# Performance work log

Hardware: AMD Instinct MI355X
Metric: run time of the kernel (lower is better)

Reference implementation:

```python
import jax, jax.numpy as jnp
import numpy as np


def setup_inputs() -> dict:
    key = jax.random.key(0)
    ks = jax.random.split(key, 6)
    B_, S, D, N = 8, 4096, 1024, 16
    return {
        "x": jax.random.normal(ks[0], (B_, S, D), dtype=jnp.float32),
        "A": jax.random.normal(ks[1], (N, N), dtype=jnp.float32),
        "B": jax.random.normal(ks[2], (D, N), dtype=jnp.float32),
        "C": jax.random.normal(ks[3], (N, D), dtype=jnp.float32),
        "W_out": jax.random.normal(ks[4], (D, D), dtype=jnp.float32) * 0.02,
        "b_out": jax.random.normal(ks[5], (D,), dtype=jnp.float32) * 0.02,
    }


def reference(x, A, B, C, W_out, b_out):
    # x: [batch, seq, d_model]. Recurrence: h_t = tanh(x_t @ B + h_{t-1} @ A.T)
    # Precompute the input projection for all timesteps (the only large GEMM),
    # then scan the tiny d_state-wide recurrence over time.
    xB = jnp.einsum("bsd,dn->sbn", x, B)  # [seq, batch, d_state]
    h0 = jnp.zeros((x.shape[0], A.shape[0]), dtype=x.dtype)

    def step(h, xb_t):
        h = jnp.tanh(xb_t + h @ A.T)
        return h, h

    _, hs = jax.lax.scan(step, h0, xB)  # hs: [seq, batch, d_state]
    y = jnp.einsum("sbn,nd->bsd", hs, C)  # [batch, seq, d_model]
    # proj_out (torch Linear): y @ W.T + b
    return y @ W_out.T + b_out
```

## Files before the change

kernel.cpp:

```cpp
#include <hip/hip_runtime.h>
#include <math.h>

#define B_DIM 8
#define S_DIM 4096
#define D_DIM 1024
#define N_DIM 16
#define ROWS (B_DIM * S_DIM)

#define CHUNK_L 32
#define WARM 64
#define STEPS (CHUNK_L + WARM)
#define NCHAIN (B_DIM * (S_DIM / CHUNK_L))

#define TILE_R 64
#define TILE_K 64
#define XB_BLOCKS (ROWS / TILE_R)
#define CW_BLOCKS ((N_DIM * D_DIM) / 256)

__global__ __launch_bounds__(256) void k_xbcw(const float* __restrict__ x,
                                              const float* __restrict__ Bm,
                                              float* __restrict__ xb,
                                              const float* __restrict__ C,
                                              const float* __restrict__ W,
                                              float* __restrict__ CW) {
    const int t = threadIdx.x;
    if (blockIdx.x >= XB_BLOCKS) {
        int u = (blockIdx.x - XB_BLOCKS) * 256 + t;
        int d = u >> 4;
        int n = u & 15;
        const float* crow = C + n * D_DIM;
        const float* wrow = W + (size_t)d * D_DIM;
        float acc = 0.f;
#pragma unroll 4
        for (int k = 0; k < D_DIM; k += 4) {
            float4 c4 = *(const float4*)(crow + k);
            float4 w4 = *(const float4*)(wrow + k);
            acc = fmaf(c4.x, w4.x, acc);
            acc = fmaf(c4.y, w4.y, acc);
            acc = fmaf(c4.z, w4.z, acc);
            acc = fmaf(c4.w, w4.w, acc);
        }
        CW[n * D_DIM + d] = acc;
        return;
    }
    __shared__ float xs[TILE_R][68];
    __shared__ float bs[TILE_K][20];
    const int row0 = blockIdx.x * TILE_R;
    const int row = t >> 2;
    const int nq = (t & 3) * 4;
    float4 acc = {0.f, 0.f, 0.f, 0.f};

    for (int kc = 0; kc < D_DIM; kc += TILE_K) {
#pragma unroll
        for (int p = 0; p < 4; ++p) {
            int fid = p * 256 + t;
            int r = fid >> 4;
            int q = (fid & 15) * 4;
            float4 v = *(const float4*)(x + (size_t)(row0 + r) * D_DIM + kc + q);
            xs[r][q + 0] = v.x; xs[r][q + 1] = v.y;
            xs[r][q + 2] = v.z; xs[r][q + 3] = v.w;
        }
        {
            int r = t >> 2;
            int q = (t & 3) * 4;
            float4 v = *(const float4*)(Bm + (size_t)(kc + r) * N_DIM + q);
            bs[r][q + 0] = v.x; bs[r][q + 1] = v.y;
            bs[r][q + 2] = v.z; bs[r][q + 3] = v.w;
        }
        __syncthreads();
#pragma unroll 8
        for (int kk = 0; kk < TILE_K; ++kk) {
            float xv = xs[row][kk];
            acc.x = fmaf(xv, bs[kk][nq + 0], acc.x);
            acc.y = fmaf(xv, bs[kk][nq + 1], acc.y);
            acc.z = fmaf(xv, bs[kk][nq + 2], acc.z);
            acc.w = fmaf(xv, bs[kk][nq + 3], acc.w);
        }
        __syncthreads();
    }
    *(float4*)(xb + (size_t)(row0 + row) * N_DIM + nq) = acc;
}

__global__ __launch_bounds__(64) void k_scan(const float* __restrict__ xb,
                                             const float* __restrict__ A,
                                             float* __restrict__ hs) {
    const int tid = threadIdx.x;
    const int n = tid & 15;
    const int base4 = (tid & 48) * 4;

    const int chain = blockIdx.x * 4 + (tid >> 4);
    const int b = chain >> 7;
    const int chunk = chain & 127;
    const int t0 = chunk * CHUNK_L - WARM;

    float Ar[16];
#pragma unroll
    for (int m4 = 0; m4 < 16; m4 += 4) {
        float4 v = *(const float4*)(A + n * 16 + m4);
        Ar[m4 + 0] = v.x; Ar[m4 + 1] = v.y; Ar[m4 + 2] = v.z; Ar[m4 + 3] = v.w;
    }

    const float* xp = xb + (size_t)b * S_DIM * N_DIM + n;
    float* hp = hs + (size_t)b * S_DIM * N_DIM + n;

    float ring[8];
#pragma unroll
    for (int i = 0; i < 8; ++i) {
        int tt = t0 + i;
        ring[i] = (tt >= 0) ? xp[(size_t)tt * N_DIM] : 0.f;
    }

    float h = 0.f;
    for (int tr0 = 0; tr0 < STEPS; tr0 += 8) {
#pragma unroll
        for (int j = 0; j < 8; ++j) {
            const int tr = tr0 + j;
            const float xv = ring[j];
            const int hbits = __float_as_int(h);
            int hm[16];
#pragma unroll
            for (int m = 0; m < 16; ++m)
                hm[m] = __builtin_amdgcn_ds_bpermute(base4 + m * 4, hbits);
            float acc0 = xv, acc1 = 0.f;
#pragma unroll
            for (int m = 0; m < 8; ++m) {
                acc0 = fmaf(Ar[m], __int_as_float(hm[m]), acc0);
                acc1 = fmaf(Ar[m + 8], __int_as_float(hm[m + 8]), acc1);
            }
            float g = acc0 + acc1;
            float ax = fabsf(g);
            float e = __expf(2.f * ax);
            float tv = 1.f - 2.f / (e + 1.f);
            h = (g < 0.f) ? -tv : tv;
            if (tr >= WARM)
                hp[(size_t)(t0 + tr) * N_DIM] = h;
            int tt = t0 + tr + 8;
            if (tr + 8 < STEPS)
                ring[j] = (tt >= 0) ? xp[(size_t)tt * N_DIM] : 0.f;
        }
    }
}

__global__ __launch_bounds__(256) void k_out(const float* __restrict__ hs,
                                             const float* __restrict__ CW,
                                             const float* __restrict__ bias,
                                             float* __restrict__ out) {
    const int t = threadIdx.x;
    const int d0 = t * 4;
    const int row0 = blockIdx.x * 32;
    float4 cw[16];
#pragma unroll
    for (int nn = 0; nn < 16; ++nn)
        cw[nn] = *(const float4*)(CW + nn * D_DIM + d0);
    float4 b4 = *(const float4*)(bias + d0);

    for (int r = row0; r < row0 + 32; ++r) {
        const float4* hp = (const float4*)(hs + (size_t)r * N_DIM);
        float4 h0 = hp[0], h1 = hp[1], h2 = hp[2], h3 = hp[3];
        float hv[16] = {h0.x, h0.y, h0.z, h0.w, h1.x, h1.y, h1.z, h1.w,
                        h2.x, h2.y, h2.z, h2.w, h3.x, h3.y, h3.z, h3.w};
        float4 acc = b4;
#pragma unroll
        for (int nn = 0; nn < 16; ++nn) {
            acc.x = fmaf(hv[nn], cw[nn].x, acc.x);
            acc.y = fmaf(hv[nn], cw[nn].y, acc.y);
            acc.z = fmaf(hv[nn], cw[nn].z, acc.z);
            acc.w = fmaf(hv[nn], cw[nn].w, acc.w);
        }
        *(float4*)(out + (size_t)r * D_DIM + d0) = acc;
    }
}

extern "C" void kernel_launch(void* const* d_in, const int* in_sizes, int n_in,
                              void* d_out, int out_size, void* d_ws,
                              size_t ws_size, hipStream_t stream) {
    const float* x    = (const float*)d_in[0];
    const float* A    = (const float*)d_in[1];
    const float* Bm   = (const float*)d_in[2];
    const float* C    = (const float*)d_in[3];
    const float* W    = (const float*)d_in[4];
    const float* bias = (const float*)d_in[5];
    float* out = (float*)d_out;

    float* ws = (float*)d_ws;
    float* xb = ws;
    float* hs = ws + 524288;
    float* CW = ws + 1048576;

    k_xbcw<<<dim3(XB_BLOCKS + CW_BLOCKS), dim3(256), 0, stream>>>(x, Bm, xb, C, W, CW);
    k_scan<<<dim3(NCHAIN / 4), dim3(64), 0, stream>>>(xb, A, hs);
    k_out<<<dim3(ROWS / 32), dim3(256), 0, stream>>>(hs, CW, bias, out);
}
```

Baseline: 121.6 us.

## Restructure x@B GEMM as split-K with register prefetch and separate reduction

The x@B projection now splits K into four quarters across blocks. Each thread owns one row and holds all 16 output columns in registers, reads B straight from global memory as broadcast loads, and prefetches the next x chunk into registers while computing the current one. Partial sums go to a workspace, and a new reduction kernel adds them into xb. The aim is more arithmetic per shared-memory load and less synchronisation than the old 64x64 tiling. The cost is an extra launch plus the write and read of the partial sums.

```diff
diff --git a/kernel.cpp b/kernel.cpp
--- a/kernel.cpp
+++ b/kernel.cpp
@@ -12,14 +12,16 @@
 #define STEPS (CHUNK_L + WARM)
 #define NCHAIN (B_DIM * (S_DIM / CHUNK_L))
 
-#define TILE_R 64
-#define TILE_K 64
-#define XB_BLOCKS (ROWS / TILE_R)
+#define XB_BLOCKS 512
 #define CW_BLOCKS ((N_DIM * D_DIM) / 256)
+#define XROWS 256
+#define KQ 256
+#define CK 32
+#define PAD 36
 
 __global__ __launch_bounds__(256) void k_xbcw(const float* __restrict__ x,
                                               const float* __restrict__ Bm,
-                                              float* __restrict__ xb,
+                                              float* __restrict__ parts,
                                               const float* __restrict__ C,
                                               const float* __restrict__ W,
                                               float* __restrict__ CW) {
@@ -43,42 +45,85 @@
         CW[n * D_DIM + d] = acc;
         return;
     }
-    __shared__ float xs[TILE_R][68];
-    __shared__ float bs[TILE_K][20];
-    const int row0 = blockIdx.x * TILE_R;
-    const int row = t >> 2;
-    const int nq = (t & 3) * 4;
-    float4 acc = {0.f, 0.f, 0.f, 0.f};
-
-    for (int kc = 0; kc < D_DIM; kc += TILE_K) {
-#pragma unroll
-        for (int p = 0; p < 4; ++p) {
+    __shared__ float xs[XROWS * PAD];
+    const int rt = blockIdx.x >> 2;
+    const int kq = blockIdx.x & 3;
+    const int row0 = rt * XROWS;
+    const int kq0 = kq * KQ;
+    const float* xbase = x + (size_t)row0 * D_DIM + kq0;
+
+    float acc[16];
+#pragma unroll
+    for (int n = 0; n < 16; ++n) acc[n] = 0.f;
+
+    float4 pf[8];
+#pragma unroll
+    for (int p = 0; p < 8; ++p) {
+        int fid = p * 256 + t;
+        int r = fid >> 3;
+        int q = fid & 7;
+        pf[p] = *(const float4*)(xbase + (size_t)r * D_DIM + q * 4);
+    }
+
+    for (int c = 0; c < 8; ++c) {
+        __syncthreads();
+#pragma unroll
+        for (int p = 0; p < 8; ++p) {
             int fid = p * 256 + t;
-            int r = fid >> 4;
-            int q = (fid & 15) * 4;
-            float4 v = *(const float4*)(x + (size_t)(row0 + r) * D_DIM + kc + q);
-            xs[r][q + 0] = v.x; xs[r][q + 1] = v.y;
-            xs[r][q + 2] = v.z; xs[r][q + 3] = v.w;
-        }
-        {
-            int r = t >> 2;
-            int q = (t & 3) * 4;
-            float4 v = *(const float4*)(Bm + (size_t)(kc + r) * N_DIM + q);
-            bs[r][q + 0] = v.x; bs[r][q + 1] = v.y;
-            bs[r][q + 2] = v.z; bs[r][q + 3] = v.w;
+            int r = fid >> 3;
+            int q = fid & 7;
+            *(float4*)(xs + r * PAD + q * 4) = pf[p];
         }
         __syncthreads();
-#pragma unroll 8
-        for (int kk = 0; kk < TILE_K; ++kk) {
-            float xv = xs[row][kk];
-            acc.x = fmaf(xv, bs[kk][nq + 0], acc.x);
-            acc.y = fmaf(xv, bs[kk][nq + 1], acc.y);
-            acc.z = fmaf(xv, bs[kk][nq + 2], acc.z);
-            acc.w = fmaf(xv, bs[kk][nq + 3], acc.w);
-        }
-        __syncthreads();
-    }
-    *(float4*)(xb + (size_t)(row0 + row) * N_DIM + nq) = acc;
+        if (c < 7) {
+#pragma unroll
+            for (int p = 0; p < 8; ++p) {
+                int fid = p * 256 + t;
+                int r = fid >> 3;
+                int q = fid & 7;
+                pf[p] = *(const float4*)(xbase + (size_t)r * D_DIM +
+                                         (c + 1) * CK + q * 4);
+            }
+        }
+        const float* bk = Bm + (size_t)(kq0 + c * CK) * N_DIM;
+#pragma unroll
+        for (int j = 0; j < 8; ++j) {
+            float4 xv = *(const float4*)(xs + t * PAD + j * 4);
+            const float* b0 = bk + (j * 4 + 0) * N_DIM;
+            const float* b1 = bk + (j * 4 + 1) * N_DIM;
+            const float* b2 = bk + (j * 4 + 2) * N_DIM;
+            const float* b3 = bk + (j * 4 + 3) * N_DIM;
+#pragma unroll
+            for (int n = 0; n < 16; ++n) {
+                float a = acc[n];
+                a = fmaf(xv.x, b0[n], a);
+                a = fmaf(xv.y, b1[n], a);
+                a = fmaf(xv.z, b2[n], a);
+                a = fmaf(xv.w, b3[n], a);
+                acc[n] = a;
+            }
+        }
+    }
+    float* op = parts + ((size_t)kq * ROWS + row0 + t) * N_DIM;
+#pragma unroll
+    for (int j = 0; j < 4; ++j) {
+        float4 v = {acc[j * 4 + 0], acc[j * 4 + 1],
+                    acc[j * 4 + 2], acc[j * 4 + 3]};
+        *(float4*)(op + j * 4) = v;
+    }
+}
+
+__global__ __launch_bounds__(256) void k_red(const float* __restrict__ parts,
+                                             float* __restrict__ xb) {
+    int i = (blockIdx.x * 256 + threadIdx.x) * 4;
+    const size_t Q = (size_t)ROWS * N_DIM;
+    float4 a = *(const float4*)(parts + i);
+    float4 b = *(const float4*)(parts + Q + i);
+    float4 c = *(const float4*)(parts + 2 * Q + i);
+    float4 d = *(const float4*)(parts + 3 * Q + i);
+    float4 s = {(a.x + b.x) + (c.x + d.x), (a.y + b.y) + (c.y + d.y),
+                (a.z + b.z) + (c.z + d.z), (a.w + b.w) + (c.w + d.w)};
+    *(float4*)(xb + i) = s;
 }
 
 __global__ __launch_bounds__(64) void k_scan(const float* __restrict__ xb,
@@ -182,12 +227,15 @@
     const float* bias = (const float*)d_in[5];
     float* out = (float*)d_out;
 
-    float* ws = (float*)d_ws;
-    float* xb = ws;
-    float* hs = ws + 524288;
-    float* CW = ws + 1048576;
-
-    k_xbcw<<<dim3(XB_BLOCKS + CW_BLOCKS), dim3(256), 0, stream>>>(x, Bm, xb, C, W, CW);
+    float* ws    = (float*)d_ws;
+    float* xb    = ws;
+    float* hs    = ws + 524288;
+    float* CW    = ws + 1048576;
+    float* parts = ws + 1064960;
+
+    k_xbcw<<<dim3(XB_BLOCKS + CW_BLOCKS), dim3(256), 0, stream>>>(
+        x, Bm, parts, C, W, CW);
+    k_red<<<dim3(ROWS * N_DIM / 1024), dim3(256), 0, stream>>>(parts, xb);
     k_scan<<<dim3(NCHAIN / 4), dim3(64), 0, stream>>>(xb, A, hs);
     k_out<<<dim3(ROWS / 32), dim3(256), 0, stream>>>(hs, CW, bias, out);
 }
```

After: 171.0 us. 40.7% more time.

## Split-K the x@B projection with register-blocked tiles and a reduction kernel

Applied to the files above, without the earlier changes.

Replaces the shared-memory tiled x@B GEMM with a split-K version. Each block handles 512 rows by 64 k. Each thread holds 8 rows by 4 outputs in registers and double-buffers its x loads straight from global memory instead of staging them through LDS. Partial sums go to a 16-way workspace, and a new reduction kernel sums them into xb. This aims to raise memory-level parallelism and FMA density for the bandwidth-bound 128MB read of x. In exchange it adds an extra launch plus about 32MB of partial-sum traffic, and the x loads are strided across rows.

```diff
diff --git a/kernel.cpp b/kernel.cpp
--- a/kernel.cpp
+++ b/kernel.cpp
@@ -12,20 +12,21 @@
 #define STEPS (CHUNK_L + WARM)
 #define NCHAIN (B_DIM * (S_DIM / CHUNK_L))
 
-#define TILE_R 64
-#define TILE_K 64
-#define XB_BLOCKS (ROWS / TILE_R)
+#define KSPLIT 16
+#define KB 64
+#define RT2 512
+#define XB2_BLOCKS ((ROWS / RT2) * KSPLIT)
 #define CW_BLOCKS ((N_DIM * D_DIM) / 256)
 
-__global__ __launch_bounds__(256) void k_xbcw(const float* __restrict__ x,
-                                              const float* __restrict__ Bm,
-                                              float* __restrict__ xb,
-                                              const float* __restrict__ C,
-                                              const float* __restrict__ W,
-                                              float* __restrict__ CW) {
+__global__ __launch_bounds__(256, 4) void k_xbcw(const float* __restrict__ x,
+                                                 const float* __restrict__ Bm,
+                                                 float* __restrict__ parts,
+                                                 const float* __restrict__ C,
+                                                 const float* __restrict__ W,
+                                                 float* __restrict__ CW) {
     const int t = threadIdx.x;
-    if (blockIdx.x >= XB_BLOCKS) {
-        int u = (blockIdx.x - XB_BLOCKS) * 256 + t;
+    if (blockIdx.x >= XB2_BLOCKS) {
+        int u = (blockIdx.x - XB2_BLOCKS) * 256 + t;
         int d = u >> 4;
         int n = u & 15;
         const float* crow = C + n * D_DIM;
@@ -43,42 +44,87 @@
         CW[n * D_DIM + d] = acc;
         return;
     }
-    __shared__ float xs[TILE_R][68];
-    __shared__ float bs[TILE_K][20];
-    const int row0 = blockIdx.x * TILE_R;
-    const int row = t >> 2;
+    __shared__ float bs[KB * N_DIM];
+    const int rt = blockIdx.x >> 4;
+    const int ks = blockIdx.x & 15;
+    const int row0 = rt * RT2;
+    const int k0 = ks * KB;
+
+    *(float4*)(bs + t * 4) = *(const float4*)(Bm + (size_t)k0 * N_DIM + t * 4);
+    __syncthreads();
+
+    const int rg = t >> 2;
     const int nq = (t & 3) * 4;
-    float4 acc = {0.f, 0.f, 0.f, 0.f};
-
-    for (int kc = 0; kc < D_DIM; kc += TILE_K) {
-#pragma unroll
-        for (int p = 0; p < 4; ++p) {
-            int fid = p * 256 + t;
-            int r = fid >> 4;
-            int q = (fid & 15) * 4;
-            float4 v = *(const float4*)(x + (size_t)(row0 + r) * D_DIM + kc + q);
-            xs[r][q + 0] = v.x; xs[r][q + 1] = v.y;
-            xs[r][q + 2] = v.z; xs[r][q + 3] = v.w;
-        }
-        {
-            int r = t >> 2;
-            int q = (t & 3) * 4;
-            float4 v = *(const float4*)(Bm + (size_t)(kc + r) * N_DIM + q);
-            bs[r][q + 0] = v.x; bs[r][q + 1] = v.y;
-            bs[r][q + 2] = v.z; bs[r][q + 3] = v.w;
-        }
-        __syncthreads();
-#pragma unroll 8
-        for (int kk = 0; kk < TILE_K; ++kk) {
-            float xv = xs[row][kk];
-            acc.x = fmaf(xv, bs[kk][nq + 0], acc.x);
-            acc.y = fmaf(xv, bs[kk][nq + 1], acc.y);
-            acc.z = fmaf(xv, bs[kk][nq + 2], acc.z);
-            acc.w = fmaf(xv, bs[kk][nq + 3], acc.w);
-        }
-        __syncthreads();
-    }
-    *(float4*)(xb + (size_t)(row0 + row) * N_DIM + nq) = acc;
+    const float* xr = x + (size_t)(row0 + rg * 8) * D_DIM + k0;
+
+    float4 acc[8];
+#pragma unroll
+    for (int i = 0; i < 8; ++i) acc[i] = {0.f, 0.f, 0.f, 0.f};
+
+    float4 bufA[8], bufB[8];
+#pragma unroll
+    for (int i = 0; i < 8; ++i)
+        bufA[i] = *(const float4*)(xr + (size_t)i * D_DIM);
+#pragma unroll
+    for (int i = 0; i < 8; ++i)
+        bufB[i] = *(const float4*)(xr + (size_t)i * D_DIM + 4);
+
+#define FMAALL(BUF, JJ)                                                    \
+    {                                                                      \
+        const float* bk = bs + (JJ) * 4 * N_DIM + nq;                      \
+        float4 b0 = *(const float4*)(bk + 0 * N_DIM);                      \
+        float4 b1 = *(const float4*)(bk + 1 * N_DIM);                      \
+        float4 b2 = *(const float4*)(bk + 2 * N_DIM);                      \
+        float4 b3 = *(const float4*)(bk + 3 * N_DIM);                      \
+        _Pragma("unroll")                                                  \
+        for (int i = 0; i < 8; ++i) {                                      \
+            float4 xv = BUF[i];                                            \
+            float4 a = acc[i];                                             \
+            a.x = fmaf(xv.x, b0.x, a.x); a.y = fmaf(xv.x, b0.y, a.y);      \
+            a.z = fmaf(xv.x, b0.z, a.z); a.w = fmaf(xv.x, b0.w, a.w);      \
+            a.x = fmaf(xv.y, b1.x, a.x); a.y = fmaf(xv.y, b1.y, a.y);      \
+            a.z = fmaf(xv.y, b1.z, a.z); a.w = fmaf(xv.y, b1.w, a.w);      \
+            a.x = fmaf(xv.z, b2.x, a.x); a.y = fmaf(xv.z, b2.y, a.y);      \
+            a.z = fmaf(xv.z, b2.z, a.z); a.w = fmaf(xv.z, b2.w, a.w);      \
+            a.x = fmaf(xv.w, b3.x, a.x); a.y = fmaf(xv.w, b3.y, a.y);      \
+            a.z = fmaf(xv.w, b3.z, a.z); a.w = fmaf(xv.w, b3.w, a.w);      \
+            acc[i] = a;                                                    \
+        }                                                                  \
+    }
+
+    for (int j = 0; j < 16; j += 2) {
+        FMAALL(bufA, j)
+        if (j + 2 < 16) {
+#pragma unroll
+            for (int i = 0; i < 8; ++i)
+                bufA[i] = *(const float4*)(xr + (size_t)i * D_DIM + (j + 2) * 4);
+        }
+        FMAALL(bufB, j + 1)
+        if (j + 3 < 16) {
+#pragma unroll
+            for (int i = 0; i < 8; ++i)
+                bufB[i] = *(const float4*)(xr + (size_t)i * D_DIM + (j + 3) * 4);
+        }
+    }
+#undef FMAALL
+
+    float* op = parts + ((size_t)ks * ROWS + row0 + rg * 8) * N_DIM + nq;
+#pragma unroll
+    for (int i = 0; i < 8; ++i)
+        *(float4*)(op + (size_t)i * N_DIM) = acc[i];
+}
+
+__global__ __launch_bounds__(256) void k_red(const float* __restrict__ parts,
+                                             float* __restrict__ xb) {
+    int i = (blockIdx.x * 256 + threadIdx.x) * 4;
+    const size_t Q = (size_t)ROWS * N_DIM;
+    float4 s = *(const float4*)(parts + i);
+#pragma unroll
+    for (int q = 1; q < KSPLIT; ++q) {
+        float4 v = *(const float4*)(parts + (size_t)q * Q + i);
+        s.x += v.x; s.y += v.y; s.z += v.z; s.w += v.w;
+    }
+    *(float4*)(xb + i) = s;
 }
 
 __global__ __launch_bounds__(64) void k_scan(const float* __restrict__ xb,
@@ -182,12 +228,15 @@
     const float* bias = (const float*)d_in[5];
     float* out = (float*)d_out;
 
-    float* ws = (float*)d_ws;
-    float* xb = ws;
-    float* hs = ws + 524288;
-    float* CW = ws + 1048576;
-
-    k_xbcw<<<dim3(XB_BLOCKS + CW_BLOCKS), dim3(256), 0, stream>>>(x, Bm, xb, C, W, CW);
+    float* ws    = (float*)d_ws;
+    float* xb    = ws;
+    float* hs    = ws + 524288;
+    float* CW    = ws + 1048576;
+    float* parts = ws + 1064960;
+
+    k_xbcw<<<dim3(XB2_BLOCKS + CW_BLOCKS), dim3(256), 0, stream>>>(
+        x, Bm, parts, C, W, CW);
+    k_red<<<dim3(ROWS * N_DIM / 1024), dim3(256), 0, stream>>>(parts, xb);
     k_scan<<<dim3(NCHAIN / 4), dim3(64), 0, stream>>>(xb, A, hs);
     k_out<<<dim3(ROWS / 32), dim3(256), 0, stream>>>(hs, CW, bias, out);
 }
```

New measurement: 388.0 us. +219.2%, slower.

## Double-buffer xB GEMM tiles with direct global-to-LDS loads and XOR swizzle

Applied to the files above, without the earlier changes.

Rewrites the x@B projection loop so x and B tiles go straight from global memory into LDS via global_load_lds, bypassing registers. Two buffers let the next k-tile load while the current one is computed. An XOR swizzle on the x tile layout avoids bank conflicts on float4 LDS reads. The aim is to hide load latency in this memory-bound GEMM. It risks a race on the async LDS writes, since only one barrier per iteration orders the prefetch against readers of the other buffer, and it doubles LDS use.

```diff
diff --git a/kernel.cpp b/kernel.cpp
--- a/kernel.cpp
+++ b/kernel.cpp
@@ -12,10 +12,15 @@
 #define STEPS (CHUNK_L + WARM)
 #define NCHAIN (B_DIM * (S_DIM / CHUNK_L))
 
-#define TILE_R 64
-#define TILE_K 64
-#define XB_BLOCKS (ROWS / TILE_R)
+#define XR 64
+#define XB_BLOCKS (ROWS / XR)
 #define CW_BLOCKS ((N_DIM * D_DIM) / 256)
+
+__device__ __forceinline__ void gl_lds16(const float* g, float* l) {
+    __builtin_amdgcn_global_load_lds(
+        (const __attribute__((address_space(1))) void*)g,
+        (__attribute__((address_space(3))) void*)l, 16, 0, 0);
+}
 
 __global__ __launch_bounds__(256) void k_xbcw(const float* __restrict__ x,
                                               const float* __restrict__ Bm,
@@ -43,41 +48,66 @@
         CW[n * D_DIM + d] = acc;
         return;
     }
-    __shared__ float xs[TILE_R][68];
-    __shared__ float bs[TILE_K][20];
-    const int row0 = blockIdx.x * TILE_R;
+    __shared__ float xs[2][XR * 64];
+    __shared__ float bsb[2][64 * N_DIM];
+    const int w = t >> 6;
+    const int l = t & 63;
+    const int lr = l >> 4;
+    const int kb = l & 15;
+    const int row0 = blockIdx.x * XR;
+
     const int row = t >> 2;
     const int nq = (t & 3) * 4;
+    const int sw = row & 7;
     float4 acc = {0.f, 0.f, 0.f, 0.f};
 
-    for (int kc = 0; kc < D_DIM; kc += TILE_K) {
-#pragma unroll
-        for (int p = 0; p < 4; ++p) {
-            int fid = p * 256 + t;
-            int r = fid >> 4;
-            int q = (fid & 15) * 4;
-            float4 v = *(const float4*)(x + (size_t)(row0 + r) * D_DIM + kc + q);
-            xs[r][q + 0] = v.x; xs[r][q + 1] = v.y;
-            xs[r][q + 2] = v.z; xs[r][q + 3] = v.w;
-        }
-        {
-            int r = t >> 2;
-            int q = (t & 3) * 4;
-            float4 v = *(const float4*)(Bm + (size_t)(kc + r) * N_DIM + q);
-            bs[r][q + 0] = v.x; bs[r][q + 1] = v.y;
-            bs[r][q + 2] = v.z; bs[r][q + 3] = v.w;
+#define STAGE(XSB, BSP, KT)                                                 \
+    {                                                                       \
+        _Pragma("unroll")                                                   \
+        for (int i = 0; i < 4; ++i) {                                       \
+            int rr = w * 16 + i * 4 + lr;                                   \
+            const float* src = x + (size_t)(row0 + rr) * D_DIM +            \
+                               (KT) * 64 + ((kb ^ (rr & 7)) * 4);           \
+            gl_lds16(src, (XSB) + (w * 16 + i * 4) * 64);                   \
+        }                                                                   \
+        const float* bsrc = Bm + (size_t)(KT) * 64 * N_DIM + w * 256 + l * 4;\
+        gl_lds16(bsrc, (BSP) + w * 256);                                    \
+    }
+
+    int cur = 0;
+    STAGE(xs[0], bsb[0], 0)
+    __syncthreads();
+
+    for (int kt = 0; kt < 16; ++kt) {
+        if (kt < 15) {
+            float* xn = xs[cur ^ 1];
+            float* bn = bsb[cur ^ 1];
+            STAGE(xn, bn, kt + 1)
+        }
+        const float* xsb = xs[cur];
+        const float* bsp = bsb[cur];
+#pragma unroll
+        for (int q = 0; q < 16; ++q) {
+            float4 xv = *(const float4*)(xsb + row * 64 + ((q ^ sw) * 4));
+            const float* bk = bsp + q * 4 * N_DIM + nq;
+            float4 b0 = *(const float4*)(bk + 0 * N_DIM);
+            float4 b1 = *(const float4*)(bk + 1 * N_DIM);
+            float4 b2 = *(const float4*)(bk + 2 * N_DIM);
+            float4 b3 = *(const float4*)(bk + 3 * N_DIM);
+            acc.x = fmaf(xv.x, b0.x, acc.x); acc.y = fmaf(xv.x, b0.y, acc.y);
+            acc.z = fmaf(xv.x, b0.z, acc.z); acc.w = fmaf(xv.x, b0.w, acc.w);
+            acc.x = fmaf(xv.y, b1.x, acc.x); acc.y = fmaf(xv.y, b1.y, acc.y);
+            acc.z = fmaf(xv.y, b1.z, acc.z); acc.w = fmaf(xv.y, b1.w, acc.w);
+            acc.x = fmaf(xv.z, b2.x, acc.x); acc.y = fmaf(xv.z, b2.y, acc.y);
+            acc.z = fmaf(xv.z, b2.z, acc.z); acc.w = fmaf(xv.z, b2.w, acc.w);
+            acc.x = fmaf(xv.w, b3.x, acc.x); acc.y = fmaf(xv.w, b3.y, acc.y);
+            acc.z = fmaf(xv.w, b3.z, acc.z); acc.w = fmaf(xv.w, b3.w, acc.w);
         }
         __syncthreads();
-#pragma unroll 8
-        for (int kk = 0; kk < TILE_K; ++kk) {
-            float xv = xs[row][kk];
-            acc.x = fmaf(xv, bs[kk][nq + 0], acc.x);
-            acc.y = fmaf(xv, bs[kk][nq + 1], acc.y);
-            acc.z = fmaf(xv, bs[kk][nq + 2], acc.z);
-            acc.w = fmaf(xv, bs[kk][nq + 3], acc.w);
-        }
-        __syncthreads();
-    }
+        cur ^= 1;
+    }
+#undef STAGE
+
     *(float4*)(xb + (size_t)(row0 + row) * N_DIM + nq) = acc;
 }
 
@@ -187,7 +217,8 @@
     float* hs = ws + 524288;
     float* CW = ws + 1048576;
 
-    k_xbcw<<<dim3(XB_BLOCKS + CW_BLOCKS), dim3(256), 0, stream>>>(x, Bm, xb, C, W, CW);
+    k_xbcw<<<dim3(XB_BLOCKS + CW_BLOCKS), dim3(256), 0, stream>>>(
+        x, Bm, xb, C, W, CW);
     k_scan<<<dim3(NCHAIN / 4), dim3(64), 0, stream>>>(xb, A, hs);
     k_out<<<dim3(ROWS / 32), dim3(256), 0, stream>>>(hs, CW, bias, out);
 }
```

After: 121.5 us. About the same (-0.0%).
